# Kernel optimization log

Hardware: AMD Instinct MI355X
Metric: run time of the kernel (lower is better)

The kernel has to match this reference:

```python
import jax, jax.numpy as jnp
import numpy as np

VOCAB = 50257
D_MODEL = 1024
BATCH = 4
SEQ = 4096


def setup_inputs() -> dict:
    key = jax.random.key(0)
    k_ids, k_w = jax.random.split(key)
    input = jax.random.randint(k_ids, (BATCH, SEQ), 0, VOCAB, dtype=jnp.int32)
    # Linear(vocab, d_model, bias=False) weight: [d_model, vocab]
    W = jax.random.normal(k_w, (D_MODEL, VOCAB), dtype=jnp.float32) * (1.0 / np.sqrt(VOCAB))
    return {"input": input, "W": W}


def reference(input, W):
    # one_hot(input, vocab) @ W.T  ==  gather columns of W
    # out[b, s, :] = W[:, input[b, s]]  -> shape [B, S, d_model]
    return jnp.take(W.T, input, axis=0)
```

## Files before the change

kernel.cpp:

```cpp
#include <hip/hip_runtime.h>
#include <stdint.h>

#define VOCAB   50257
#define DMODEL  1024
#define VWIN    256
#define NB      ((VOCAB + VWIN - 1) / VWIN)
#define DCHUNK  32
#define HBLK    16
#define NTOT    (NB * HBLK)

#define WS_COUNT  0
#define WS_START  4096
#define WS_PERM   8192

__global__ __launch_bounds__(256) void hist_kernel(
    const int* __restrict__ ids, int* __restrict__ ws, int n_tokens)
{
    __shared__ int h[NB];
    const int tid = threadIdx.x, blk = blockIdx.x;
    for (int i = tid; i < NB; i += 256) h[i] = 0;
    __syncthreads();
    const int per = (n_tokens + HBLK - 1) / HBLK;
    const int t0 = blk * per;
    const int t1 = min(n_tokens, t0 + per);
    for (int t = t0 + tid; t < t1; t += 256)
        atomicAdd(&h[ids[t] >> 8], 1);
    __syncthreads();
    for (int i = tid; i < NB; i += 256)
        ws[WS_COUNT + i * HBLK + blk] = h[i];
}

__global__ __launch_bounds__(256) void scan_kernel(int* __restrict__ ws)
{
    __shared__ int s[256];
    const int tid = threadIdx.x;
    const int CH = (NTOT + 255) / 256;
    const int base = tid * CH;
    int vals[(NTOT + 255) / 256];
    int sum = 0;
#pragma unroll
    for (int j = 0; j < CH; j++) {
        int idx = base + j;
        int v = (idx < NTOT) ? ws[WS_COUNT + idx] : 0;
        vals[j] = v; sum += v;
    }
    s[tid] = sum;
    __syncthreads();
    for (int off = 1; off < 256; off <<= 1) {
        int v = (tid >= off) ? s[tid - off] : 0;
        __syncthreads();
        s[tid] += v;
        __syncthreads();
    }
    int run = (tid > 0) ? s[tid - 1] : 0;
#pragma unroll
    for (int j = 0; j < CH; j++) {
        int idx = base + j;
        if (idx < NTOT) ws[WS_START + idx] = run;
        run += vals[j];
    }
    if (tid == 255) ws[WS_START + NTOT] = run;
}

__global__ __launch_bounds__(256) void scatter_kernel(
    const int* __restrict__ ids, int* __restrict__ ws, int n_tokens)
{
    __shared__ int cur[NB];
    const int tid = threadIdx.x, blk = blockIdx.x;
    for (int i = tid; i < NB; i += 256)
        cur[i] = ws[WS_START + i * HBLK + blk];
    __syncthreads();
    const int per = (n_tokens + HBLK - 1) / HBLK;
    const int t0 = blk * per;
    const int t1 = min(n_tokens, t0 + per);
    for (int t = t0 + tid; t < t1; t += 256) {
        int id = ids[t];
        int b  = id >> 8;
        int pos = atomicAdd(&cur[b], 1);
        ws[WS_PERM + pos] = (int)(((uint32_t)id << 16) | (uint32_t)t);
    }
}

__global__ __launch_bounds__(256) void emit_kernel(
    const float* __restrict__ W, const int* __restrict__ ws,
    float* __restrict__ out)
{
    __shared__ float tile[DCHUNK][VWIN + 1];

    const int vwin = blockIdx.x;
    const int d0   = blockIdx.y * DCHUNK;
    const int v0   = vwin << 8;
    const int tid  = threadIdx.x;

    const float* Wbase = W + (size_t)d0 * VOCAB + v0;
    const int limit = VOCAB - v0;
    if (limit >= VWIN) {
        for (int e = tid * 4; e < DCHUNK * VWIN; e += 256 * 4) {
            int r = e >> 8, c = e & 255;
            float4 v = *(const float4*)(Wbase + (size_t)r * VOCAB + c);
            tile[r][c]     = v.x;
            tile[r][c + 1] = v.y;
            tile[r][c + 2] = v.z;
            tile[r][c + 3] = v.w;
        }
    } else {
        for (int e = tid * 4; e < DCHUNK * VWIN; e += 256 * 4) {
            int r = e >> 8, c = e & 255;
#pragma unroll
            for (int j = 0; j < 4; j++)
                tile[r][c + j] = (c + j < limit)
                    ? Wbase[(size_t)r * VOCAB + c + j] : 0.0f;
        }
    }
    __syncthreads();

    const int begin = ws[WS_START + vwin * HBLK];
    const int end   = ws[WS_START + (vwin + 1) * HBLK];
    const int lane  = tid & 63;
    const int w     = tid >> 6;
    const int g     = lane >> 3;
    const int dsub  = (lane & 7) << 2;

    for (int i = begin + w * 8; i < end; i += 32) {
        int idx = i + g;
        if (idx < end) {
            uint32_t packed = (uint32_t)ws[WS_PERM + idx];
            int t   = (int)(packed & 0xFFFFu);
            int col = (int)(packed >> 16) - v0;
            float4 v;
            v.x = tile[dsub][col];
            v.y = tile[dsub + 1][col];
            v.z = tile[dsub + 2][col];
            v.w = tile[dsub + 3][col];
            *(float4*)(out + (size_t)t * DMODEL + d0 + dsub) = v;
        }
    }
}

extern "C" void kernel_launch(void* const* d_in, const int* in_sizes, int n_in,
                              void* d_out, int out_size, void* d_ws, size_t ws_size,
                              hipStream_t stream) {
    const int*   ids = (const int*)d_in[0];
    const float* W   = (const float*)d_in[1];
    float*       out = (float*)d_out;
    int*         ws  = (int*)d_ws;

    const int n_tokens = in_sizes[0];

    hist_kernel<<<HBLK, 256, 0, stream>>>(ids, ws, n_tokens);
    scan_kernel<<<1, 256, 0, stream>>>(ws);
    scatter_kernel<<<HBLK, 256, 0, stream>>>(ids, ws, n_tokens);

    dim3 grid(NB, DMODEL / DCHUNK);
    emit_kernel<<<grid, 256, 0, stream>>>(W, ws, out);
}
```

Measured before the change: 320.1 us.

## Double-buffer W tiles via async global-to-LDS loads across d-chunks

The emit kernel now has each block loop over eight 32-row d-chunks instead of one, so the grid shrinks from 32 to 4 blocks along d. Loading of the next W tile into a second LDS buffer uses asynchronous global_load_lds and is issued while the current tile is gathered into the output. The goal is to hide W load latency behind the output scatter and to reuse the per-window token index reads across chunks. In exchange, LDS use per block doubles and there are far fewer blocks in flight, which could hurt latency hiding. The tail vocab window keeps a slow scalar, non-overlapped path.

```diff
diff --git a/kernel.cpp b/kernel.cpp
--- a/kernel.cpp
+++ b/kernel.cpp
@@ -6,12 +6,16 @@
 #define VWIN    256
 #define NB      ((VOCAB + VWIN - 1) / VWIN)
 #define DCHUNK  32
+#define NCHUNK  8
 #define HBLK    16
 #define NTOT    (NB * HBLK)
 
 #define WS_COUNT  0
 #define WS_START  4096
 #define WS_PERM   8192
+
+typedef __attribute__((address_space(1))) const void glb_cv;
+typedef __attribute__((address_space(3))) void lds_v;
 
 __global__ __launch_bounds__(256) void hist_kernel(
     const int* __restrict__ ids, int* __restrict__ ws, int n_tokens)
@@ -85,54 +89,74 @@
     const float* __restrict__ W, const int* __restrict__ ws,
     float* __restrict__ out)
 {
-    __shared__ float tile[DCHUNK][VWIN + 1];
+    __shared__ float tile[2][DCHUNK][VWIN + 1];
 
     const int vwin = blockIdx.x;
-    const int d0   = blockIdx.y * DCHUNK;
+    const int q    = blockIdx.y;
     const int v0   = vwin << 8;
     const int tid  = threadIdx.x;
-
-    const float* Wbase = W + (size_t)d0 * VOCAB + v0;
-    const int limit = VOCAB - v0;
-    if (limit >= VWIN) {
-        for (int e = tid * 4; e < DCHUNK * VWIN; e += 256 * 4) {
-            int r = e >> 8, c = e & 255;
-            float4 v = *(const float4*)(Wbase + (size_t)r * VOCAB + c);
-            tile[r][c]     = v.x;
-            tile[r][c + 1] = v.y;
-            tile[r][c + 2] = v.z;
-            tile[r][c + 3] = v.w;
-        }
-    } else {
-        for (int e = tid * 4; e < DCHUNK * VWIN; e += 256 * 4) {
-            int r = e >> 8, c = e & 255;
-#pragma unroll
-            for (int j = 0; j < 4; j++)
-                tile[r][c + j] = (c + j < limit)
-                    ? Wbase[(size_t)r * VOCAB + c + j] : 0.0f;
-        }
-    }
-    __syncthreads();
+    const int lane = tid & 63;
+    const int w    = tid >> 6;
 
     const int begin = ws[WS_START + vwin * HBLK];
     const int end   = ws[WS_START + (vwin + 1) * HBLK];
-    const int lane  = tid & 63;
-    const int w     = tid >> 6;
-    const int g     = lane >> 3;
-    const int dsub  = (lane & 7) << 2;
 
-    for (int i = begin + w * 8; i < end; i += 32) {
-        int idx = i + g;
-        if (idx < end) {
-            uint32_t packed = (uint32_t)ws[WS_PERM + idx];
-            int t   = (int)(packed & 0xFFFFu);
-            int col = (int)(packed >> 16) - v0;
-            float4 v;
-            v.x = tile[dsub][col];
-            v.y = tile[dsub + 1][col];
-            v.z = tile[dsub + 2][col];
-            v.w = tile[dsub + 3][col];
-            *(float4*)(out + (size_t)t * DMODEL + d0 + dsub) = v;
+    const int g    = lane >> 3;
+    const int dsub = (lane & 7) << 2;
+
+    auto stage_async = [&](int c, int b) {
+        const int dbase = q * 256 + c * DCHUNK;
+        const float* rowbase = W + (size_t)(dbase + w * 8) * VOCAB + v0;
+#pragma unroll
+        for (int rr = 0; rr < 8; rr++) {
+            const float* rowp = rowbase + (size_t)rr * VOCAB;
+#pragma unroll
+            for (int qq = 0; qq < 4; qq++) {
+                __builtin_amdgcn_global_load_lds(
+                    (glb_cv*)(rowp + qq * 64 + lane),
+                    (lds_v*)&tile[b][w * 8 + rr][qq * 64],
+                    4, 0, 0);
+            }
+        }
+    };
+
+    auto emit_chunk = [&](int c, int b) {
+        const int dout = q * 256 + c * DCHUNK;
+        for (int i = begin + w * 8; i < end; i += 32) {
+            int idx = i + g;
+            if (idx < end) {
+                uint32_t packed = (uint32_t)ws[WS_PERM + idx];
+                int t   = (int)(packed & 0xFFFFu);
+                int col = (int)(packed >> 16) - v0;
+                float4 v;
+                v.x = tile[b][dsub][col];
+                v.y = tile[b][dsub + 1][col];
+                v.z = tile[b][dsub + 2][col];
+                v.w = tile[b][dsub + 3][col];
+                *(float4*)(out + (size_t)t * DMODEL + dout + dsub) = v;
+            }
+        }
+    };
+
+    if (vwin < NB - 1) {
+        stage_async(0, 0);
+        __syncthreads();
+        for (int c = 0; c < NCHUNK; c++) {
+            const int b = c & 1;
+            if (c + 1 < NCHUNK) stage_async(c + 1, b ^ 1);
+            emit_chunk(c, b);
+            __syncthreads();
+        }
+    } else {
+        const int limit = VOCAB - v0;
+        for (int c = 0; c < NCHUNK; c++) {
+            const int dbase = q * 256 + c * DCHUNK;
+            for (int r = 0; r < DCHUNK; r++)
+                for (int col = tid; col < limit; col += 256)
+                    tile[0][r][col] = W[(size_t)(dbase + r) * VOCAB + v0 + col];
+            __syncthreads();
+            emit_chunk(c, 0);
+            __syncthreads();
         }
     }
 }
@@ -151,6 +175,6 @@
     scan_kernel<<<1, 256, 0, stream>>>(ws);
     scatter_kernel<<<HBLK, 256, 0, stream>>>(ids, ws, n_tokens);
 
-    dim3 grid(NB, DMODEL / DCHUNK);
+    dim3 grid(NB, 4);
     emit_kernel<<<grid, 256, 0, stream>>>(W, ws, out);
 }
```

Measured after the change: 410.1 us. 28.1% more time.
